# Kernel tuning notes

Hardware: AMD Instinct MI355X
Metric: run time of the kernel (lower is better)

The kernel has to match this reference:

```python
import jax, jax.numpy as jnp
import numpy as np

D_MODEL = 1024
N_HEADS = 16
HEAD_DIM = D_MODEL // N_HEADS
D_FF = 4 * D_MODEL
EPS = 1e-5


def _layer_norm(h, g, b):
    m = jnp.mean(h, axis=-1, keepdims=True)
    v = jnp.mean(jnp.square(h - m), axis=-1, keepdims=True)
    return (h - m) * jax.lax.rsqrt(v + EPS) * g + b


def setup_inputs() -> dict:
    key = jax.random.key(0)
    ks = jax.random.split(key, 10)
    B, S, D = 4, 2048, D_MODEL
    scale = 0.02
    inp = {
        "x": jax.random.normal(ks[0], (B, S, D), dtype=jnp.float32),
        "Wq": scale * jax.random.normal(ks[1], (D, D), dtype=jnp.float32),
        "Wk": scale * jax.random.normal(ks[2], (D, D), dtype=jnp.float32),
        "Wv": scale * jax.random.normal(ks[3], (D, D), dtype=jnp.float32),
        "Wo": scale * jax.random.normal(ks[4], (D, D), dtype=jnp.float32),
        "ln1_g": jnp.ones((D,), dtype=jnp.float32),
        "ln1_b": jnp.zeros((D,), dtype=jnp.float32),
        "ln2_g": jnp.ones((D,), dtype=jnp.float32),
        "ln2_b": jnp.zeros((D,), dtype=jnp.float32),
        "W1": scale * jax.random.normal(ks[5], (D, D_FF), dtype=jnp.float32),
        "b1": jnp.zeros((D_FF,), dtype=jnp.float32),
        "W2": scale * jax.random.normal(ks[6], (D_FF, D), dtype=jnp.float32),
        "b2": jnp.zeros((D,), dtype=jnp.float32),
        "Wc": scale * jax.random.normal(ks[7], (D, 1), dtype=jnp.float32),
        "bc": jnp.zeros((1,), dtype=jnp.float32),
    }
    return inp


def reference(x, Wq, Wk, Wv, Wo, ln1_g, ln1_b, ln2_g, ln2_b, W1, b1, W2, b2, Wc, bc):
    B, S, D = x.shape
    H, hd = N_HEADS, HEAD_DIM
    # --- causal self-attention (pre-LN) ---
    h = _layer_norm(x, ln1_g, ln1_b)
    q = (h @ Wq).reshape(B, S, H, hd).transpose(0, 2, 1, 3)  # [B,H,S,hd]
    k = (h @ Wk).reshape(B, S, H, hd).transpose(0, 2, 1, 3)
    v = (h @ Wv).reshape(B, S, H, hd).transpose(0, 2, 1, 3)
    scores = jnp.einsum("bhqd,bhkd->bhqk", q, k) / jnp.sqrt(jnp.asarray(hd, x.dtype))
    causal = jnp.triu(jnp.ones((S, S), dtype=bool), k=1)
    scores = jnp.where(causal[None, None, :, :], -jnp.inf, scores)
    attn = jax.nn.softmax(scores, axis=-1)
    ctx = jnp.einsum("bhqk,bhkd->bhqd", attn, v).transpose(0, 2, 1, 3).reshape(B, S, D)
    x1 = x + ctx @ Wo
    # --- FFN (pre-LN, ReLU) ---
    h2 = _layer_norm(x1, ln2_g, ln2_b)
    ff = jax.nn.relu(h2 @ W1 + b1) @ W2 + b2
    x_out = x1 + ff
    # --- adaptive confidence gate: mean-pool seq -> Linear -> sigmoid -> batch mean ---
    pooled = jnp.mean(x_out, axis=1)  # [B,D]
    conf = jnp.mean(jax.nn.sigmoid(pooled @ Wc + bc), axis=0)  # [1]
    return x_out, conf
```

## Files before the change

kernel.cpp:

```cpp
#include <hip/hip_runtime.h>
#include <hip/hip_bf16.h>

typedef __hip_bfloat16 bf16;
typedef __attribute__((ext_vector_type(8))) short short8;
typedef __attribute__((ext_vector_type(4))) float f32x4;

#define D_MODELC 1024
#define D_FFC    4096
#define NHEADS   16
#define HDIM     64
#define SEQLEN   2048
#define BATCHN   4
#define MTOT     (BATCHN * SEQLEN)

__device__ __forceinline__ void async16(void* lds, const void* g) {
  __builtin_amdgcn_global_load_lds(
      (const __attribute__((address_space(1))) unsigned int*)g,
      (__attribute__((address_space(3))) unsigned int*)lds, 16, 0, 0);
}

__global__ __launch_bounds__(256) void transpose_bf16_k(
    const float* __restrict__ src, bf16* __restrict__ dst, int R, int C, float scale) {
  __shared__ float tile[32][33];
  int tx = threadIdx.x & 31, ty = threadIdx.x >> 5;
  int r0 = blockIdx.y * 32, c0 = blockIdx.x * 32;
#pragma unroll
  for (int i = 0; i < 4; i++) {
    int r = ty + i * 8;
    tile[r][tx] = src[(size_t)(r0 + r) * C + c0 + tx];
  }
  __syncthreads();
#pragma unroll
  for (int i = 0; i < 4; i++) {
    int c = ty + i * 8;
    dst[(size_t)(c0 + c) * R + r0 + tx] = __float2bfloat16(tile[tx][c] * scale);
  }
}

__global__ __launch_bounds__(256) void ln_bf16_k(
    const float* __restrict__ x, const float* __restrict__ g,
    const float* __restrict__ b, bf16* __restrict__ out) {
  int row = blockIdx.x;
  int t = threadIdx.x;
  f32x4 v = ((const f32x4*)(x + (size_t)row * D_MODELC))[t];
  float s = v[0] + v[1] + v[2] + v[3];
  float ss = v[0] * v[0] + v[1] * v[1] + v[2] * v[2] + v[3] * v[3];
#pragma unroll
  for (int m = 1; m < 64; m <<= 1) {
    s += __shfl_xor(s, m);
    ss += __shfl_xor(ss, m);
  }
  __shared__ float red[8];
  int w = t >> 6, l = t & 63;
  if (l == 0) { red[w] = s; red[4 + w] = ss; }
  __syncthreads();
  s = red[0] + red[1] + red[2] + red[3];
  ss = red[4] + red[5] + red[6] + red[7];
  float mean = s * (1.0f / D_MODELC);
  float var = ss * (1.0f / D_MODELC) - mean * mean;
  float rs = rsqrtf(var + 1e-5f);
  f32x4 gv = ((const f32x4*)g)[t];
  f32x4 bv = ((const f32x4*)b)[t];
  unsigned short u[4];
#pragma unroll
  for (int j = 0; j < 4; j++) {
    float o = (v[j] - mean) * rs * gv[j] + bv[j];
    u[j] = __bfloat16_as_ushort(__float2bfloat16(o));
  }
  unsigned int lo = (unsigned int)u[0] | ((unsigned int)u[1] << 16);
  unsigned int hi = (unsigned int)u[2] | ((unsigned int)u[3] << 16);
  ((uint2*)(out + (size_t)row * D_MODELC))[t] = make_uint2(lo, hi);
}

enum { EPI_QKV = 0, EPI_RESID = 1, EPI_BIAS_RELU = 2, EPI_BIAS_RESID = 3 };

template <int EPI>
__device__ __forceinline__ void epi_write(
    int gm, int gn, float v, int N,
    const float* __restrict__ bias, const float* __restrict__ resid,
    float* __restrict__ outF, bf16* __restrict__ outB) {
  if constexpr (EPI == EPI_QKV) {
    int sel = gn >> 10, d = gn & 1023;
    int b_ = gm >> 11, s_ = gm & 2047;
    int h2 = d >> 6, dd = d & 63;
    size_t bh = (size_t)b_ * NHEADS + h2;
    size_t dst;
    if (sel < 2) {
      dst = (size_t)sel * ((size_t)MTOT * D_MODELC) + (bh * SEQLEN + s_) * HDIM + dd;
    } else {
      dst = 2 * ((size_t)MTOT * D_MODELC) + (bh * HDIM + dd) * SEQLEN + s_;
    }
    outB[dst] = __float2bfloat16(v);
  } else if constexpr (EPI == EPI_RESID) {
    size_t idx = (size_t)gm * N + gn;
    outF[idx] = resid[idx] + v;
  } else if constexpr (EPI == EPI_BIAS_RELU) {
    float z = v + bias[gn];
    outB[(size_t)gm * N + gn] = __float2bfloat16(z > 0.f ? z : 0.f);
  } else {
    size_t idx = (size_t)gm * N + gn;
    outF[idx] = resid[idx] + v + bias[gn];
  }
}

#define BM 128
#define BN 128
#define BKK 64

template <int EPI>
__global__ __launch_bounds__(256) void gemm_nt(
    const bf16* __restrict__ A, const bf16* __restrict__ BT, int M, int N, int K,
    const float* __restrict__ bias, const float* __restrict__ resid,
    float* __restrict__ outF, bf16* __restrict__ outB) {
  __shared__ bf16 As[BM * BKK];
  __shared__ bf16 Bs[BN * BKK];
  const int t = threadIdx.x;
  const int l = t & 63;
  const int w = t >> 6;
  const int wm = w >> 1, wn = w & 1;

  int nwg = gridDim.x * gridDim.y;
  int bid = blockIdx.y * gridDim.x + blockIdx.x;
  if ((nwg & 7) == 0) {
    int q8 = nwg >> 3;
    bid = (bid & 7) * q8 + (bid >> 3);
  }
  const int bx = bid % gridDim.x, by = bid / gridDim.x;
  const int m0 = by * BM, n0 = bx * BN;
  const int lr = l & 15, lkg = l >> 4;

  f32x4 acc[4][4];
#pragma unroll
  for (int i = 0; i < 4; i++)
#pragma unroll
    for (int j = 0; j < 4; j++) acc[i][j] = (f32x4){0.f, 0.f, 0.f, 0.f};

  const char* Abase = (const char*)(A + (size_t)m0 * K);
  const char* Bbase = (const char*)(BT + (size_t)n0 * K);

  for (int k0 = 0; k0 < K; k0 += BKK) {
#pragma unroll
    for (int c = 0; c < 4; c++) {
      int off = (c * 256 + t) * 16;
      int r = off >> 7;
      int sg = ((off >> 4) & 7) ^ (r & 7);
      async16((char*)As + off, Abase + ((size_t)r * K + k0) * 2 + sg * 16);
      async16((char*)Bs + off, Bbase + ((size_t)r * K + k0) * 2 + sg * 16);
    }
    __syncthreads();
    short8 a[2][4], b[2][4];
#pragma unroll
    for (int kk = 0; kk < 2; kk++) {
#pragma unroll
      for (int mi = 0; mi < 4; mi++) {
        int row = wm * 64 + mi * 16 + lr;
        int sl = (kk * 4 + lkg) ^ (row & 7);
        a[kk][mi] = *(const short8*)((const char*)As + row * 128 + sl * 16);
      }
#pragma unroll
      for (int ni = 0; ni < 4; ni++) {
        int row = wn * 64 + ni * 16 + lr;
        int sl = (kk * 4 + lkg) ^ (row & 7);
        b[kk][ni] = *(const short8*)((const char*)Bs + row * 128 + sl * 16);
      }
    }
#pragma unroll
    for (int kk = 0; kk < 2; kk++)
#pragma unroll
      for (int mi = 0; mi < 4; mi++)
#pragma unroll
        for (int ni = 0; ni < 4; ni++)
          acc[mi][ni] = __builtin_amdgcn_mfma_f32_16x16x32_bf16(a[kk][mi], b[kk][ni], acc[mi][ni], 0, 0, 0);
    __syncthreads();
  }

#pragma unroll
  for (int mi = 0; mi < 4; mi++)
#pragma unroll
    for (int ni = 0; ni < 4; ni++)
#pragma unroll
      for (int j = 0; j < 4; j++) {
        int gm = m0 + wm * 64 + mi * 16 + lkg * 4 + j;
        int gn = n0 + wn * 64 + ni * 16 + lr;
        epi_write<EPI>(gm, gn, acc[mi][ni][j], N, bias, resid, outF, outB);
      }
}

#define KVB 64
#define QB2 128
#define PSTR 76

__global__ __launch_bounds__(256) void attn_k(
    const bf16* __restrict__ qg, const bf16* __restrict__ kg,
    const bf16* __restrict__ vtg, bf16* __restrict__ ctx) {
  const int bid = blockIdx.x;
  const int qt = (SEQLEN / QB2 - 1) - (bid >> 6);
  const int bh = bid & 63;
  const int q0 = qt * QB2;
  const int t = threadIdx.x, w = t >> 6, l = t & 63;
  const int lr = l & 15, lkg = l >> 4, lk = lkg * 8;

  const bf16* Q  = qg  + (size_t)bh * SEQLEN * HDIM;
  const bf16* Kg = kg  + (size_t)bh * SEQLEN * HDIM;
  const bf16* Vt = vtg + (size_t)bh * HDIM * SEQLEN;

  __shared__ bf16 Ks[KVB * PSTR];
  __shared__ bf16 Vs[HDIM * PSTR];
  __shared__ bf16 Ps[4][16 * PSTR];

  short8 qf[2][2];
#pragma unroll
  for (int mi = 0; mi < 2; mi++)
#pragma unroll
    for (int kk = 0; kk < 2; kk++)
      qf[mi][kk] = *(const short8*)&Q[(size_t)(q0 + w * 32 + mi * 16 + lr) * HDIM + kk * 32 + lk];

  const short8 bones = {0x3F80, 0x3F80, 0x3F80, 0x3F80, 0x3F80, 0x3F80, 0x3F80, 0x3F80};

  f32x4 o[2][4];
  f32x4 ol[2];
#pragma unroll
  for (int mi = 0; mi < 2; mi++) {
    ol[mi] = (f32x4){0.f, 0.f, 0.f, 0.f};
#pragma unroll
    for (int nh = 0; nh < 4; nh++) o[mi][nh] = (f32x4){0.f, 0.f, 0.f, 0.f};
  }

  const int srow = t >> 3;
  const int scc  = (t & 7) * 8;

  const int ntiles = 2 * qt + 2;
  for (int tkv = 0; tkv < ntiles; tkv++) {
    const int kv0 = tkv * KVB;
#pragma unroll
    for (int r = 0; r < 2; r++) {
      int row = srow + r * 32;
      short8 kv = *(const short8*)&Kg[(size_t)(kv0 + row) * HDIM + scc];
      *(short8*)&Ks[row * PSTR + scc] = kv;
      short8 vv = *(const short8*)&Vt[(size_t)row * SEQLEN + kv0 + scc];
      *(short8*)&Vs[row * PSTR + scc] = vv;
    }
    __syncthreads();

    const bool active = (kv0 <= q0 + w * 32 + 31);
    if (active) {
      short8 kf[4][2];
#pragma unroll
      for (int ni = 0; ni < 4; ni++)
#pragma unroll
        for (int kk = 0; kk < 2; kk++)
          kf[ni][kk] = *(const short8*)&Ks[(ni * 16 + lr) * PSTR + kk * 32 + lk];
      f32x4 s[2][4];
#pragma unroll
      for (int mi = 0; mi < 2; mi++)
#pragma unroll
        for (int ni = 0; ni < 4; ni++) {
          f32x4 a = (f32x4){0.f, 0.f, 0.f, 0.f};
#pragma unroll
          for (int kk = 0; kk < 2; kk++)
            a = __builtin_amdgcn_mfma_f32_16x16x32_bf16(qf[mi][kk], kf[ni][kk], a, 0, 0, 0);
          s[mi][ni] = a;
        }
      if (tkv >= ntiles - 2) {
#pragma unroll
        for (int mi = 0; mi < 2; mi++)
#pragma unroll
          for (int ni = 0; ni < 4; ni++)
#pragma unroll
            for (int j = 0; j < 4; j++) {
              int qq = q0 + w * 32 + mi * 16 + lkg * 4 + j;
              int kv = kv0 + ni * 16 + lr;
              if (kv > qq) s[mi][ni][j] = -1e30f;
            }
      }
#pragma unroll
      for (int mi = 0; mi < 2; mi++) {
#pragma unroll
        for (int ni = 0; ni < 4; ni++)
#pragma unroll
          for (int j = 0; j < 4; j++)
            ((short*)Ps[w])[(lkg * 4 + j) * PSTR + ni * 16 + lr] =
                (short)__bfloat16_as_ushort(__float2bfloat16(exp2f(s[mi][ni][j])));
#pragma unroll
        for (int kk = 0; kk < 2; kk++) {
          short8 pa = *(const short8*)&Ps[w][lr * PSTR + kk * 32 + lk];
          ol[mi] = __builtin_amdgcn_mfma_f32_16x16x32_bf16(pa, bones, ol[mi], 0, 0, 0);
#pragma unroll
          for (int nh = 0; nh < 4; nh++) {
            short8 vb = *(const short8*)&Vs[(nh * 16 + lr) * PSTR + kk * 32 + lk];
            o[mi][nh] = __builtin_amdgcn_mfma_f32_16x16x32_bf16(pa, vb, o[mi][nh], 0, 0, 0);
          }
        }
      }
    }
    __syncthreads();
  }

  const int b_ = bh >> 4, h_ = bh & 15;
#pragma unroll
  for (int mi = 0; mi < 2; mi++)
#pragma unroll
    for (int j = 0; j < 4; j++) {
      float inv = 1.0f / ol[mi][j];
      int qq = q0 + w * 32 + mi * 16 + lkg * 4 + j;
      size_t base = (((size_t)b_ * SEQLEN + qq) * NHEADS + h_) * HDIM;
#pragma unroll
      for (int nh = 0; nh < 4; nh++)
        ctx[base + nh * 16 + lr] = __float2bfloat16(o[mi][nh][j] * inv);
    }
}

__global__ __launch_bounds__(256) void pool_partial_k(
    const float* __restrict__ xo, float* __restrict__ part) {
  int blk = blockIdx.x;
  int b_ = blk >> 4, ch = blk & 15;
  int t = threadIdx.x;
  f32x4 acc = (f32x4){0.f, 0.f, 0.f, 0.f};
  const float* base = xo + ((size_t)b_ * SEQLEN + (size_t)ch * 128) * D_MODELC;
  for (int r = 0; r < 128; r++)
    acc += ((const f32x4*)(base + (size_t)r * D_MODELC))[t];
  ((f32x4*)(part + (size_t)blk * D_MODELC))[t] = acc;
}

__global__ __launch_bounds__(256) void conf_k(
    const float* __restrict__ part, const float* __restrict__ Wc,
    const float* __restrict__ bc, float* __restrict__ outc) {
  int t = threadIdx.x;
  __shared__ float red[4];
  float total = 0.f;
  for (int b_ = 0; b_ < BATCHN; b_++) {
    f32x4 sum = (f32x4){0.f, 0.f, 0.f, 0.f};
    for (int ch = 0; ch < 16; ch++)
      sum += ((const f32x4*)(part + (size_t)(b_ * 16 + ch) * D_MODELC))[t];
    f32x4 wv = ((const f32x4*)Wc)[t];
    float d = (sum[0] * wv[0] + sum[1] * wv[1] + sum[2] * wv[2] + sum[3] * wv[3]) * (1.0f / SEQLEN);
#pragma unroll
    for (int m = 1; m < 64; m <<= 1) d += __shfl_xor(d, m);
    int wq = t >> 6, l = t & 63;
    if (l == 0) red[wq] = d;
    __syncthreads();
    float z = red[0] + red[1] + red[2] + red[3] + bc[0];
    total += 1.0f / (1.0f + __expf(-z));
    __syncthreads();
  }
  if (t == 0) outc[0] = total * (1.0f / BATCHN);
}

extern "C" void kernel_launch(void* const* d_in, const int* in_sizes, int n_in,
                              void* d_out, int out_size, void* d_ws, size_t ws_size,
                              hipStream_t stream) {
  const float* x    = (const float*)d_in[0];
  const float* Wq   = (const float*)d_in[1];
  const float* Wk   = (const float*)d_in[2];
  const float* Wv   = (const float*)d_in[3];
  const float* Wo   = (const float*)d_in[4];
  const float* ln1g = (const float*)d_in[5];
  const float* ln1b = (const float*)d_in[6];
  const float* ln2g = (const float*)d_in[7];
  const float* ln2b = (const float*)d_in[8];
  const float* W1   = (const float*)d_in[9];
  const float* b1   = (const float*)d_in[10];
  const float* W2   = (const float*)d_in[11];
  const float* b2   = (const float*)d_in[12];
  const float* Wc   = (const float*)d_in[13];
  const float* bc   = (const float*)d_in[14];

  char* ws = (char*)d_ws;
  const size_t MB = 1024 * 1024;
  bf16* qkv   = (bf16*)(ws);
  bf16* ctx   = (bf16*)(ws + 48 * MB);
  bf16* ff1   = (bf16*)(ws);
  bf16* h     = (bf16*)(ws + 64 * MB);
  bf16* WqkvT = (bf16*)(ws + 80 * MB);
  bf16* WoT   = (bf16*)(ws + 86 * MB);
  bf16* W1T   = (bf16*)(ws + 88 * MB);
  bf16* W2T   = (bf16*)(ws + 96 * MB);
  float* part = (float*)(ws + 104 * MB);

  float* xout = (float*)d_out;
  dim3 blk(256);

  const float SCL2 = 0.125f * 1.44269504f;

  transpose_bf16_k<<<dim3(32, 32), blk, 0, stream>>>(Wq, WqkvT, 1024, 1024, SCL2);
  transpose_bf16_k<<<dim3(32, 32), blk, 0, stream>>>(Wk, WqkvT + 1024 * 1024, 1024, 1024, 1.0f);
  transpose_bf16_k<<<dim3(32, 32), blk, 0, stream>>>(Wv, WqkvT + 2 * 1024 * 1024, 1024, 1024, 1.0f);
  transpose_bf16_k<<<dim3(32, 32), blk, 0, stream>>>(Wo, WoT, 1024, 1024, 1.0f);
  transpose_bf16_k<<<dim3(128, 32), blk, 0, stream>>>(W1, W1T, 1024, 4096, 1.0f);
  transpose_bf16_k<<<dim3(32, 128), blk, 0, stream>>>(W2, W2T, 4096, 1024, 1.0f);

  ln_bf16_k<<<MTOT, blk, 0, stream>>>(x, ln1g, ln1b, h);
  gemm_nt<EPI_QKV><<<dim3(3072 / BN, MTOT / BM), blk, 0, stream>>>(
      h, WqkvT, MTOT, 3072, 1024, nullptr, nullptr, nullptr, qkv);
  attn_k<<<dim3((SEQLEN / QB2) * 64), blk, 0, stream>>>(
      qkv, qkv + (size_t)MTOT * D_MODELC, qkv + 2 * (size_t)MTOT * D_MODELC, ctx);
  gemm_nt<EPI_RESID><<<dim3(1024 / BN, MTOT / BM), blk, 0, stream>>>(
      ctx, WoT, MTOT, 1024, 1024, nullptr, x, xout, nullptr);
  ln_bf16_k<<<MTOT, blk, 0, stream>>>(xout, ln2g, ln2b, h);
  gemm_nt<EPI_BIAS_RELU><<<dim3(4096 / BN, MTOT / BM), blk, 0, stream>>>(
      h, W1T, MTOT, 4096, 1024, b1, nullptr, nullptr, ff1);
  gemm_nt<EPI_BIAS_RESID><<<dim3(1024 / BN, MTOT / BM), blk, 0, stream>>>(
      ff1, W2T, MTOT, 1024, 4096, b2, xout, xout, nullptr);
  pool_partial_k<<<64, blk, 0, stream>>>(xout, part);
  conf_k<<<1, blk, 0, stream>>>(part, Wc, bc, xout + (size_t)MTOT * D_MODELC);
}
```

Baseline: 411.7 us.

## Add 256x256 8-wave pipelined GEMM for QKV and FFN1 projections

Adds a new 512-thread GEMM with 256x256 output tiles and double-buffered LDS. Each K tile is split into four phases that interleave async global-to-LDS loads with MFMA work, using explicit waitcnt, barriers and setprio. Block IDs are remapped across eight groups for L2 locality. It replaces the older gemm_nt for the QKV and W1 projections to raise arithmetic intensity and hide load latency, at the cost of more registers and LDS and fewer blocks per launch.

```diff
diff --git a/kernel.cpp b/kernel.cpp
--- a/kernel.cpp
+++ b/kernel.cpp
@@ -184,6 +184,124 @@
         int gn = n0 + wn * 64 + ni * 16 + lr;
         epi_write<EPI>(gm, gn, acc[mi][ni][j], N, bias, resid, outF, outB);
       }
+}
+
+#define G8M 256
+#define G8N 256
+#define G8K 64
+
+template <int EPI>
+__global__ __launch_bounds__(512) void gemm8p(
+    const bf16* __restrict__ A, const bf16* __restrict__ BT, int N, int K,
+    const float* __restrict__ bias, const float* __restrict__ resid,
+    float* __restrict__ outF, bf16* __restrict__ outB) {
+  __shared__ bf16 As[2][2][G8M * 32];
+  __shared__ bf16 Bs[2][2][G8N * 32];
+  const int t = threadIdx.x;
+  const int l = t & 63, wid = t >> 6;
+  const int wr = wid >> 2, wc = wid & 3;
+  const int lr = l & 15, lkg = l >> 4;
+
+  int nwg = gridDim.x;
+  int bid = blockIdx.x;
+  int sb = (bid & 7) * (nwg >> 3) + (bid >> 3);
+  const int by = sb & 31, bx = sb >> 5;
+  const int m0 = by * G8M, n0 = bx * G8N;
+
+  const char* Abase = (const char*)(A + (size_t)m0 * K);
+  const char* Bbase = (const char*)(BT + (size_t)n0 * K);
+  const int NT = K >> 6;
+
+  f32x4 acc[8][4];
+#pragma unroll
+  for (int i = 0; i < 8; i++)
+#pragma unroll
+    for (int j = 0; j < 4; j++) acc[i][j] = (f32x4){0.f, 0.f, 0.f, 0.f};
+
+  int aoff[2][4], boff[4];
+#pragma unroll
+  for (int mih = 0; mih < 2; mih++)
+#pragma unroll
+    for (int mi = 0; mi < 4; mi++) {
+      int row = wr * 128 + (mih * 4 + mi) * 16 + lr;
+      aoff[mih][mi] = row * 64 + ((lkg ^ (row & 3)) * 16);
+    }
+#pragma unroll
+  for (int ni = 0; ni < 4; ni++) {
+    int row = wc * 64 + ni * 16 + lr;
+    boff[ni] = row * 64 + ((lkg ^ (row & 3)) * 16);
+  }
+
+#define STG8(arr, gbase, buf, kh, k0)                                          \
+  do {                                                                         \
+    _Pragma("unroll")                                                          \
+    for (int ld = 0; ld < 2; ld++) {                                           \
+      int off = (ld * 512 + t) * 16;                                           \
+      int r = off >> 6;                                                        \
+      int sg = ((off >> 4) & 3) ^ (r & 3);                                     \
+      async16((char*)arr[buf][kh] + off,                                       \
+              gbase + ((size_t)r * K + (k0) + (kh) * 32) * 2 + sg * 16);       \
+    }                                                                          \
+  } while (0)
+
+  STG8(As, Abase, 0, 0, 0);
+  STG8(Bs, Bbase, 0, 0, 0);
+  STG8(As, Abase, 0, 1, 0);
+  STG8(Bs, Bbase, 0, 1, 0);
+  asm volatile("s_waitcnt vmcnt(0)" ::: "memory");
+  __syncthreads();
+
+  for (int kt = 0; kt < NT; kt++) {
+    const int cb = kt & 1;
+    const int kn = (kt + 1 < NT) ? (kt + 1) * G8K : 0;
+#pragma unroll
+    for (int ph = 0; ph < 4; ph++) {
+      const int kh = ph >> 1, mih = ph & 1;
+      const char* Ap = (const char*)As[cb][kh];
+      const char* Bp = (const char*)Bs[cb][kh];
+      short8 a[4], b[4];
+#pragma unroll
+      for (int mi = 0; mi < 4; mi++) a[mi] = *(const short8*)(Ap + aoff[mih][mi]);
+#pragma unroll
+      for (int ni = 0; ni < 4; ni++) b[ni] = *(const short8*)(Bp + boff[ni]);
+      if (ph == 0) {
+        STG8(As, Abase, cb ^ 1, 0, kn);
+      } else if (ph == 1) {
+        STG8(Bs, Bbase, cb ^ 1, 0, kn);
+      } else if (ph == 2) {
+        STG8(As, Abase, cb ^ 1, 1, kn);
+      } else {
+        STG8(Bs, Bbase, cb ^ 1, 1, kn);
+      }
+      if (ph & 1) asm volatile("s_waitcnt vmcnt(4)" ::: "memory");
+      __builtin_amdgcn_s_barrier();
+      asm volatile("s_waitcnt lgkmcnt(0)" ::: "memory");
+      __builtin_amdgcn_sched_barrier(0);
+      __builtin_amdgcn_s_setprio(1);
+#pragma unroll
+      for (int mi = 0; mi < 4; mi++)
+#pragma unroll
+        for (int ni = 0; ni < 4; ni++)
+          acc[mih * 4 + mi][ni] = __builtin_amdgcn_mfma_f32_16x16x32_bf16(
+              a[mi], b[ni], acc[mih * 4 + mi][ni], 0, 0, 0);
+      __builtin_amdgcn_s_setprio(0);
+      __builtin_amdgcn_s_barrier();
+    }
+  }
+#undef STG8
+
+#pragma unroll
+  for (int I = 0; I < 8; I++) {
+    int rowoff = (I >> 2) * 64 + (I & 3) * 16;
+#pragma unroll
+    for (int ni = 0; ni < 4; ni++)
+#pragma unroll
+      for (int j = 0; j < 4; j++) {
+        int gm = m0 + wr * 128 + rowoff + lkg * 4 + j;
+        int gn = n0 + wc * 64 + ni * 16 + lr;
+        epi_write<EPI>(gm, gn, acc[I][ni][j], N, bias, resid, outF, outB);
+      }
+  }
 }
 
 #define KVB 64
@@ -379,6 +497,7 @@
 
   float* xout = (float*)d_out;
   dim3 blk(256);
+  dim3 blk512(512);
 
   const float SCL2 = 0.125f * 1.44269504f;
 
@@ -390,15 +509,15 @@
   transpose_bf16_k<<<dim3(32, 128), blk, 0, stream>>>(W2, W2T, 4096, 1024, 1.0f);
 
   ln_bf16_k<<<MTOT, blk, 0, stream>>>(x, ln1g, ln1b, h);
-  gemm_nt<EPI_QKV><<<dim3(3072 / BN, MTOT / BM), blk, 0, stream>>>(
-      h, WqkvT, MTOT, 3072, 1024, nullptr, nullptr, nullptr, qkv);
+  gemm8p<EPI_QKV><<<dim3((3072 / G8N) * 32), blk512, 0, stream>>>(
+      h, WqkvT, 3072, 1024, nullptr, nullptr, nullptr, qkv);
   attn_k<<<dim3((SEQLEN / QB2) * 64), blk, 0, stream>>>(
       qkv, qkv + (size_t)MTOT * D_MODELC, qkv + 2 * (size_t)MTOT * D_MODELC, ctx);
   gemm_nt<EPI_RESID><<<dim3(1024 / BN, MTOT / BM), blk, 0, stream>>>(
       ctx, WoT, MTOT, 1024, 1024, nullptr, x, xout, nullptr);
   ln_bf16_k<<<MTOT, blk, 0, stream>>>(xout, ln2g, ln2b, h);
-  gemm_nt<EPI_BIAS_RELU><<<dim3(4096 / BN, MTOT / BM), blk, 0, stream>>>(
-      h, W1T, MTOT, 4096, 1024, b1, nullptr, nullptr, ff1);
+  gemm8p<EPI_BIAS_RELU><<<dim3((4096 / G8N) * 32), blk512, 0, stream>>>(
+      h, W1T, 4096, 1024, b1, nullptr, nullptr, ff1);
   gemm_nt<EPI_BIAS_RESID><<<dim3(1024 / BN, MTOT / BM), blk, 0, stream>>>(
       ff1, W2T, MTOT, 1024, 4096, b2, xout, xout, nullptr);
   pool_partial_k<<<64, blk, 0, stream>>>(xout, part);
```

After: 486.1 us. 18.1% more time.
